# Performance work log

Hardware: AMD Instinct MI355X
Metric: run time of the kernel (lower is better)

Reference implementation:

```python
import jax, jax.numpy as jnp
from jax import lax
import numpy as np

B, N_PER = 4, 8192          # equal-sized point clouds
RATIO, K = 0.5, 16
C_IN, C_OUT = 64, 128
M_PER = int(N_PER * RATIO)  # FPS samples per cloud
BN_EPS = 1e-5


def setup_inputs() -> dict:
    key = jax.random.key(0)
    k1, k2, k3 = jax.random.split(key, 3)
    N = B * N_PER
    x = jax.random.normal(k1, (N, C_IN), jnp.float32)
    pos = jax.random.uniform(k2, (N, 3), jnp.float32)
    batch = jnp.repeat(jnp.arange(B, dtype=jnp.int32), N_PER)
    W = jax.random.normal(k3, (C_IN, C_OUT), jnp.float32) / np.sqrt(C_IN).astype(np.float32)
    b = jnp.zeros((C_OUT,), jnp.float32)
    gamma = jnp.ones((C_OUT,), jnp.float32)
    beta = jnp.zeros((C_OUT,), jnp.float32)
    return {"x": x, "pos": pos, "batch": batch, "W": W, "b": b, "gamma": gamma, "beta": beta}


def _fps_single(pos_b):
    # Deterministic farthest point sampling on one cloud [N_PER, 3] -> [M_PER] indices.
    n = pos_b.shape[0]
    def step(carry, _):
        dists, last = carry
        d = jnp.sum((pos_b - pos_b[last]) ** 2, axis=-1)
        dists = jnp.minimum(dists, d)
        nxt = jnp.argmax(dists).astype(jnp.int32)
        return (dists, nxt), nxt
    init = (jnp.full((n,), jnp.inf, pos_b.dtype), jnp.int32(0))
    _, idx = lax.scan(step, init, None, length=M_PER - 1)
    return jnp.concatenate([jnp.zeros((1,), jnp.int32), idx])


def reference(x, pos, batch, W, b, gamma, beta):
    # batch is assumed to be B contiguous equal segments of N_PER points.
    pos_b = pos.reshape(B, N_PER, 3)
    samp = jax.vmap(_fps_single)(pos_b)                                # [B, M_PER]
    new_pos = jnp.take_along_axis(pos_b, samp[:, :, None], axis=1)     # [B, M_PER, 3]

    # kNN of each sampled point among all points of the same cloud (squared L2).
    sq_p = jnp.sum(pos_b * pos_b, axis=-1)                              # [B, N_PER]
    sq_q = jnp.sum(new_pos * new_pos, axis=-1)                          # [B, M_PER]
    d2 = sq_q[:, :, None] + sq_p[:, None, :] - 2.0 * jnp.einsum('bmd,bnd->bmn', new_pos, pos_b)
    _, nbr = lax.top_k(-d2, K)                                          # [B, M_PER, K]

    # MLP: Linear -> BatchNorm1d (batch stats over all N points) -> exact GELU.
    h = x @ W + b                                                       # [N, C_OUT]
    mean = jnp.mean(h, axis=0)
    var = jnp.var(h, axis=0)
    h = (h - mean) / jnp.sqrt(var + BN_EPS) * gamma + beta
    h = jax.nn.gelu(h, approximate=False)

    h_b = h.reshape(B, N_PER, C_OUT)
    gathered = jax.vmap(lambda hb, nb: hb[nb])(h_b, nbr)                # [B, M_PER, K, C_OUT]
    new_x = jnp.max(gathered, axis=2)                                   # scatter-max == max over k neighbors

    new_batch = jnp.repeat(jnp.arange(B, dtype=batch.dtype), M_PER)
    return new_x.reshape(B * M_PER, C_OUT), new_pos.reshape(B * M_PER, 3), new_batch
```

## Files before the change

kernel.cpp:

```cpp
#include <hip/hip_runtime.h>
#include <math.h>

#define NB    4
#define NPER  8192
#define MPER  4096
#define NTOT  32768
#define MTOT  16384
#define COUT  128

#define NEWPOS_OFF 2097152
#define NEWB_OFF   2146304

#define WS_H     0u
#define WS_SQP   16777216u
#define WS_SAMP  16908288u
#define WS_PART  16973824u
#define WS_PART2 17006592u
#define WS_STAT  17039360u

__global__ void misc_kernel(const float* __restrict__ pos, float* __restrict__ sqp,
                            float* __restrict__ out) {
  int g = blockIdx.x * 1024 + threadIdx.x;
  if (g < NTOT) {
    float x = pos[g * 3 + 0], y = pos[g * 3 + 1], z = pos[g * 3 + 2];
    sqp[g] = fmaf(z, z, fmaf(x, x, __fmul_rn(y, y)));
  }
  if (g < MTOT) out[NEWB_OFF + g] = (float)(g >> 12);
}

__global__ __launch_bounds__(256) void matmul_kernel(const float* __restrict__ x,
                                                     const float* __restrict__ W,
                                                     const float* __restrict__ bias,
                                                     float* __restrict__ h) {
  __shared__ float xs[16][64];
  const int tid = threadIdx.x;
  const int rowbase = blockIdx.x * 16;
  for (int i = tid; i < 16 * 64; i += 256) xs[i >> 6][i & 63] = x[rowbase * 64 + i];
  __syncthreads();
  const int col = tid & 127;
  const int rs = (tid >> 7) * 8;
  float acc[8] = {0.f, 0.f, 0.f, 0.f, 0.f, 0.f, 0.f, 0.f};
  for (int k = 0; k < 64; ++k) {
    float wv = W[k * 128 + col];
#pragma unroll
    for (int r = 0; r < 8; ++r) acc[r] = fmaf(xs[rs + r][k], wv, acc[r]);
  }
  float bb = bias[col];
#pragma unroll
  for (int r = 0; r < 8; ++r) h[(rowbase + rs + r) * 128 + col] = acc[r] + bb;
}

__global__ __launch_bounds__(256) void stats_kernel(const float* __restrict__ h,
                                                    float* __restrict__ part,
                                                    float* __restrict__ part2) {
  const int tid = threadIdx.x;
  const int col = tid & 127;
  const int half = tid >> 7;
  const int r0 = blockIdx.x * 512;
  float s = 0.f, s2 = 0.f;
  for (int r = r0 + half; r < r0 + 512; r += 2) {
    float v = h[r * 128 + col];
    s += v;
    s2 = fmaf(v, v, s2);
  }
  __shared__ float ps[2][128], ps2[2][128];
  ps[half][col] = s;
  ps2[half][col] = s2;
  __syncthreads();
  if (half == 0) {
    part[blockIdx.x * 128 + col] = ps[0][col] + ps[1][col];
    part2[blockIdx.x * 128 + col] = ps2[0][col] + ps2[1][col];
  }
}

__global__ void finalize_kernel(const float* __restrict__ part,
                                const float* __restrict__ part2,
                                float* __restrict__ stat) {
  int col = threadIdx.x;
  float s = 0.f, s2 = 0.f;
  for (int i = 0; i < 64; ++i) {
    s += part[i * 128 + col];
    s2 += part2[i * 128 + col];
  }
  float mean = s / 32768.0f;
  float var = s2 / 32768.0f - mean * mean;
  float invstd = 1.0f / sqrtf(var + 1e-5f);
  stat[col] = mean;
  stat[128 + col] = invstd;
}

__global__ __launch_bounds__(256) void bngelu_kernel(float* __restrict__ h,
                                                     const float* __restrict__ stat,
                                                     const float* __restrict__ gamma,
                                                     const float* __restrict__ beta) {
  int base = blockIdx.x * 2048 + threadIdx.x;
#pragma unroll
  for (int t = 0; t < 8; ++t) {
    int g = base + t * 256;
    int col = g & 127;
    float v = h[g];
    float z = (v - stat[col]) * stat[128 + col];
    z = z * gamma[col] + beta[col];
    float ge = 0.5f * z * (1.0f + erff(z * 0.70710678118654752440f));
    h[g] = ge;
  }
}

#define UMAXU(a, b) (((a) > (b)) ? (a) : (b))
#define UMINU(a, b) (((a) < (b)) ? (a) : (b))
#define DPP_FMAX(m, CTRL)                                                       \
  {                                                                             \
    int t_ = __builtin_amdgcn_update_dpp(__float_as_int(m), __float_as_int(m),  \
                                         (CTRL), 0xf, 0xf, false);              \
    m = fmaxf(m, __int_as_float(t_));                                           \
  }
#define DPP_UMIN(c, CTRL)                                                       \
  {                                                                             \
    unsigned int t_ = (unsigned int)__builtin_amdgcn_update_dpp(                \
        (int)(c), (int)(c), (CTRL), 0xf, 0xf, false);                           \
    c = UMINU(c, t_);                                                           \
  }
#define FPS_DECL(i) float px##i, py##i, pz##i, dd##i;
#define FPS_LOAD(i)                     \
  {                                     \
    const int n = tid + (i) * 512;      \
    px##i = p[n * 3 + 0];               \
    py##i = p[n * 3 + 1];               \
    pz##i = p[n * 3 + 2];               \
    dd##i = INFINITY;                   \
    lpxy[n] = make_float2(px##i, py##i);\
    lpz[n] = pz##i;                     \
  }
#define FPS_PIN(i) \
  asm volatile("" : "+v"(px##i), "+v"(py##i), "+v"(pz##i));
#define FPS_DIST(i)                                                             \
  {                                                                             \
    float dx = __fsub_rn(px##i, lx), dy = __fsub_rn(py##i, ly),                 \
          dz = __fsub_rn(pz##i, lz);                                            \
    float d = fmaf(dz, dz, fmaf(dx, dx, __fmul_rn(dy, dy)));                    \
    float nd = fminf(dd##i, d);                                                 \
    dd##i = nd;                                                                 \
    m = fmaxf(m, nd);                                                           \
  }
#define FPS_MATCH(i)                                                            \
  ci = (dd##i == D) ? (unsigned int)(tid + (i) * 512) : ci;

__global__ __launch_bounds__(512)
__attribute__((amdgpu_waves_per_eu(2, 2)))
void fps_kernel(const float* __restrict__ pos,
                int* __restrict__ samp,
                float* __restrict__ out) {
  const int b = blockIdx.x;
  const int tid = threadIdx.x;
  const int wv = tid >> 6;
  const float* p = pos + b * NPER * 3;
  __shared__ float2 lpxy[NPER];
  __shared__ float lpz[NPER];
  __shared__ __align__(16) unsigned int slotD[8];
  __shared__ __align__(16) unsigned int slotI[8];
  FPS_DECL(0) FPS_DECL(1) FPS_DECL(2) FPS_DECL(3)
  FPS_DECL(4) FPS_DECL(5) FPS_DECL(6) FPS_DECL(7)
  FPS_DECL(8) FPS_DECL(9) FPS_DECL(10) FPS_DECL(11)
  FPS_DECL(12) FPS_DECL(13) FPS_DECL(14) FPS_DECL(15)
  FPS_LOAD(0) FPS_LOAD(1) FPS_LOAD(2) FPS_LOAD(3)
  FPS_LOAD(4) FPS_LOAD(5) FPS_LOAD(6) FPS_LOAD(7)
  FPS_LOAD(8) FPS_LOAD(9) FPS_LOAD(10) FPS_LOAD(11)
  FPS_LOAD(12) FPS_LOAD(13) FPS_LOAD(14) FPS_LOAD(15)
  FPS_PIN(0) FPS_PIN(1) FPS_PIN(2) FPS_PIN(3)
  FPS_PIN(4) FPS_PIN(5) FPS_PIN(6) FPS_PIN(7)
  FPS_PIN(8) FPS_PIN(9) FPS_PIN(10) FPS_PIN(11)
  FPS_PIN(12) FPS_PIN(13) FPS_PIN(14) FPS_PIN(15)
  float lx = p[0], ly = p[1], lz = p[2];
  if (tid == 0) {
    samp[b * MPER] = 0;
    out[NEWPOS_OFF + (b * MPER) * 3 + 0] = lx;
    out[NEWPOS_OFF + (b * MPER) * 3 + 1] = ly;
    out[NEWPOS_OFF + (b * MPER) * 3 + 2] = lz;
  }
  __syncthreads();
  for (int s = 1; s < MPER; ++s) {
    float m = 0.0f;
    FPS_DIST(0) FPS_DIST(1) FPS_DIST(2) FPS_DIST(3)
    FPS_DIST(4) FPS_DIST(5) FPS_DIST(6) FPS_DIST(7)
    FPS_DIST(8) FPS_DIST(9) FPS_DIST(10) FPS_DIST(11)
    FPS_DIST(12) FPS_DIST(13) FPS_DIST(14) FPS_DIST(15)
    DPP_FMAX(m, 0x111)
    DPP_FMAX(m, 0x112)
    DPP_FMAX(m, 0x114)
    DPP_FMAX(m, 0x118)
    DPP_FMAX(m, 0x142)
    DPP_FMAX(m, 0x143)
    if ((tid & 63) == 63) slotD[wv] = __float_as_uint(m);
    __syncthreads();
    const uint4* spD = (const uint4*)slotD;
    uint4 a0 = spD[0], a1 = spD[1];
    unsigned int r0 = UMAXU(UMAXU(a0.x, a0.y), UMAXU(a0.z, a0.w));
    unsigned int r1 = UMAXU(UMAXU(a1.x, a1.y), UMAXU(a1.z, a1.w));
    const float D = __uint_as_float(UMAXU(r0, r1));
    unsigned int ci = 0xFFFFFFFFu;
    FPS_MATCH(15) FPS_MATCH(14) FPS_MATCH(13) FPS_MATCH(12)
    FPS_MATCH(11) FPS_MATCH(10) FPS_MATCH(9) FPS_MATCH(8)
    FPS_MATCH(7) FPS_MATCH(6) FPS_MATCH(5) FPS_MATCH(4)
    FPS_MATCH(3) FPS_MATCH(2) FPS_MATCH(1) FPS_MATCH(0)
    DPP_UMIN(ci, 0x111)
    DPP_UMIN(ci, 0x112)
    DPP_UMIN(ci, 0x114)
    DPP_UMIN(ci, 0x118)
    DPP_UMIN(ci, 0x142)
    DPP_UMIN(ci, 0x143)
    if ((tid & 63) == 63) slotI[wv] = ci;
    __syncthreads();
    const uint4* spI = (const uint4*)slotI;
    uint4 b0 = spI[0], b1 = spI[1];
    unsigned int i0 = UMINU(UMINU(b0.x, b0.y), UMINU(b0.z, b0.w));
    unsigned int i1 = UMINU(UMINU(b1.x, b1.y), UMINU(b1.z, b1.w));
    const int widx = (int)UMINU(i0, i1);
    float2 wxy = lpxy[widx];
    float wz = lpz[widx];
    lx = wxy.x; ly = wxy.y; lz = wz;
    if (tid == 0) {
      samp[b * MPER + s] = widx;
      out[NEWPOS_OFF + (b * MPER + s) * 3 + 0] = lx;
      out[NEWPOS_OFF + (b * MPER + s) * 3 + 1] = ly;
      out[NEWPOS_OFF + (b * MPER + s) * 3 + 2] = lz;
    }
  }
}

__global__ __launch_bounds__(256) void knn_kernel(const float* __restrict__ pos,
                                                  const float* __restrict__ sqp,
                                                  const int* __restrict__ samp,
                                                  const float* __restrict__ h,
                                                  float* __restrict__ out) {
  const int q = blockIdx.x;
  const int b = q >> 12;
  const int tid = threadIdx.x;
  const int gbase = b * NPER;
  __shared__ float dist[NPER];
  __shared__ unsigned long long slot[2];
  __shared__ int nbr[16];
  const int sidx = samp[q];
  const float qx = pos[(gbase + sidx) * 3 + 0];
  const float qy = pos[(gbase + sidx) * 3 + 1];
  const float qz = pos[(gbase + sidx) * 3 + 2];
  const float sqq = sqp[gbase + sidx];
  if (tid == 0) {
    slot[0] = ~0ull;
    slot[1] = ~0ull;
  }
  unsigned long long lkey = ~0ull;
  for (int i = 0; i < 32; ++i) {
    int n = tid + i * 256;
    int g = gbase + n;
    float dot = fmaf(qz, pos[g * 3 + 2],
                     fmaf(qy, pos[g * 3 + 1], __fmul_rn(qx, pos[g * 3 + 0])));
    float d2 = __fsub_rn(__fadd_rn(sqq, sqp[g]), __fmul_rn(2.0f, dot));
    dist[n] = d2;
    unsigned int ub = __float_as_uint(d2);
    ub = (ub & 0x80000000u) ? ~ub : (ub | 0x80000000u);
    unsigned long long key = ((unsigned long long)ub << 32) | (unsigned int)n;
    lkey = (key < lkey) ? key : lkey;
  }
  __syncthreads();
  for (int r = 0; r < 16; ++r) {
    unsigned long long wk = lkey;
#pragma unroll
    for (int off = 1; off < 64; off <<= 1) {
      unsigned long long o = __shfl_xor(wk, off, 64);
      wk = (o < wk) ? o : wk;
    }
    if ((tid & 63) == 0) atomicMin(&slot[r & 1], wk);
    __syncthreads();
    unsigned long long w = slot[r & 1];
    int n = (int)(unsigned int)(w & 0xFFFFFFFFull);
    if (tid == 0) {
      nbr[r] = n;
      slot[(r & 1) ^ 1] = ~0ull;
    }
    if (tid == (n & 255)) {
      dist[n] = INFINITY;
      lkey = ~0ull;
      for (int i = 0; i < 32; ++i) {
        int nn = tid + i * 256;
        unsigned int ub = __float_as_uint(dist[nn]);
        ub = (ub & 0x80000000u) ? ~ub : (ub | 0x80000000u);
        unsigned long long kk = ((unsigned long long)ub << 32) | (unsigned int)nn;
        lkey = (kk < lkey) ? kk : lkey;
      }
    }
    __syncthreads();
  }
  if (tid < COUT) {
    float mx = -INFINITY;
#pragma unroll
    for (int r = 0; r < 16; ++r) mx = fmaxf(mx, h[(gbase + nbr[r]) * 128 + tid]);
    out[q * 128 + tid] = mx;
  }
}

extern "C" void kernel_launch(void* const* d_in, const int* in_sizes, int n_in,
                              void* d_out, int out_size, void* d_ws, size_t ws_size,
                              hipStream_t stream) {
  (void)in_sizes; (void)n_in; (void)out_size; (void)ws_size;
  const float* x     = (const float*)d_in[0];
  const float* pos   = (const float*)d_in[1];
  const float* W     = (const float*)d_in[3];
  const float* bias  = (const float*)d_in[4];
  const float* gamma = (const float*)d_in[5];
  const float* beta  = (const float*)d_in[6];
  float* out = (float*)d_out;
  char* ws = (char*)d_ws;
  float* h     = (float*)(ws + WS_H);
  float* sqp   = (float*)(ws + WS_SQP);
  int*   samp  = (int*)(ws + WS_SAMP);
  float* part  = (float*)(ws + WS_PART);
  float* part2 = (float*)(ws + WS_PART2);
  float* stat  = (float*)(ws + WS_STAT);

  misc_kernel<<<dim3(32), dim3(1024), 0, stream>>>(pos, sqp, out);
  matmul_kernel<<<dim3(2048), dim3(256), 0, stream>>>(x, W, bias, h);
  stats_kernel<<<dim3(64), dim3(256), 0, stream>>>(h, part, part2);
  finalize_kernel<<<dim3(1), dim3(128), 0, stream>>>(part, part2, stat);
  bngelu_kernel<<<dim3(2048), dim3(256), 0, stream>>>(h, stat, gamma, beta);
  fps_kernel<<<dim3(NB), dim3(512), 0, stream>>>(pos, samp, out);
  knn_kernel<<<dim3(MTOT), dim3(256), 0, stream>>>(pos, sqp, samp, h, out);
}
```

Baseline: 3.743 ms.

## Use DPP wave reductions and double-buffered slots in kNN top-k selection

```diff
diff --git a/kernel.cpp b/kernel.cpp
--- a/kernel.cpp
+++ b/kernel.cpp
@@ -227,6 +227,18 @@
   }
 }
 
+#define DPP_KMIN64(lo, hi, CTRL)                                                \
+  {                                                                             \
+    unsigned int a_ = (unsigned int)__builtin_amdgcn_update_dpp(                \
+        (int)(lo), (int)(lo), (CTRL), 0xf, 0xf, false);                         \
+    unsigned int b_ = (unsigned int)__builtin_amdgcn_update_dpp(                \
+        (int)(hi), (int)(hi), (CTRL), 0xf, 0xf, false);                         \
+    unsigned long long nk_ = ((unsigned long long)b_ << 32) | a_;               \
+    unsigned long long ok_ = ((unsigned long long)(hi) << 32) | (lo);           \
+    bool t_ = nk_ < ok_;                                                        \
+    lo = t_ ? a_ : (lo); hi = t_ ? b_ : (hi);                                   \
+  }
+
 __global__ __launch_bounds__(256) void knn_kernel(const float* __restrict__ pos,
                                                   const float* __restrict__ sqp,
                                                   const int* __restrict__ samp,
@@ -235,19 +247,15 @@
   const int q = blockIdx.x;
   const int b = q >> 12;
   const int tid = threadIdx.x;
+  const int wv = tid >> 6;
   const int gbase = b * NPER;
   __shared__ float dist[NPER];
-  __shared__ unsigned long long slot[2];
-  __shared__ int nbr[16];
+  __shared__ __align__(16) unsigned long long ckey[2][4];
   const int sidx = samp[q];
   const float qx = pos[(gbase + sidx) * 3 + 0];
   const float qy = pos[(gbase + sidx) * 3 + 1];
   const float qz = pos[(gbase + sidx) * 3 + 2];
   const float sqq = sqp[gbase + sidx];
-  if (tid == 0) {
-    slot[0] = ~0ull;
-    slot[1] = ~0ull;
-  }
   unsigned long long lkey = ~0ull;
   for (int i = 0; i < 32; ++i) {
     int n = tid + i * 256;
@@ -262,21 +270,27 @@
     lkey = (key < lkey) ? key : lkey;
   }
   __syncthreads();
+  float mx = -INFINITY;
   for (int r = 0; r < 16; ++r) {
-    unsigned long long wk = lkey;
-#pragma unroll
-    for (int off = 1; off < 64; off <<= 1) {
-      unsigned long long o = __shfl_xor(wk, off, 64);
-      wk = (o < wk) ? o : wk;
-    }
-    if ((tid & 63) == 0) atomicMin(&slot[r & 1], wk);
+    const int pr = r & 1;
+    unsigned int klo = (unsigned int)lkey;
+    unsigned int khi = (unsigned int)(lkey >> 32);
+    DPP_KMIN64(klo, khi, 0x111)
+    DPP_KMIN64(klo, khi, 0x112)
+    DPP_KMIN64(klo, khi, 0x114)
+    DPP_KMIN64(klo, khi, 0x118)
+    DPP_KMIN64(klo, khi, 0x142)
+    DPP_KMIN64(klo, khi, 0x143)
+    if ((tid & 63) == 63)
+      ckey[pr][wv] = ((unsigned long long)khi << 32) | klo;
     __syncthreads();
-    unsigned long long w = slot[r & 1];
-    int n = (int)(unsigned int)(w & 0xFFFFFFFFull);
-    if (tid == 0) {
-      nbr[r] = n;
-      slot[(r & 1) ^ 1] = ~0ull;
-    }
+    const ulonglong2* cp = (const ulonglong2*)ckey[pr];
+    ulonglong2 c0 = cp[0], c1 = cp[1];
+    unsigned long long k0 = (c0.x < c0.y) ? c0.x : c0.y;
+    unsigned long long k1 = (c1.x < c1.y) ? c1.x : c1.y;
+    k0 = (k1 < k0) ? k1 : k0;
+    const int n = (int)(unsigned int)(k0 & 0xFFFFFFFFull);
+    if (tid < COUT) mx = fmaxf(mx, h[(gbase + n) * 128 + tid]);
     if (tid == (n & 255)) {
       dist[n] = INFINITY;
       lkey = ~0ull;
@@ -288,14 +302,8 @@
         lkey = (kk < lkey) ? kk : lkey;
       }
     }
-    __syncthreads();
-  }
-  if (tid < COUT) {
-    float mx = -INFINITY;
-#pragma unroll
-    for (int r = 0; r < 16; ++r) mx = fmaxf(mx, h[(gbase + nbr[r]) * 128 + tid]);
-    out[q * 128 + tid] = mx;
-  }
+  }
+  if (tid < COUT) out[q * 128 + tid] = mx;
 }
 
 extern "C" void kernel_launch(void* const* d_in, const int* in_sizes, int n_in,
```

Result: no change. 3.695 ms (-1.3%).
